# Optimization experiments

Measured on AMD Instinct MI355X. Metric: run time of the kernel, lower is better.

Reference implementation:

```python
import jax, jax.numpy as jnp
import numpy as np
import math

D_MODEL = 1024
N_HEADS = 16
D_K = D_MODEL // N_HEADS
LN_EPS = 1e-5


def _linear_params(key, d_in, d_out):
    # torch Linear stores weight as [out, in]; xavier_uniform init
    bound = math.sqrt(6.0 / (d_in + d_out))
    kw, kb = jax.random.split(key)
    W = jax.random.uniform(kw, (d_out, d_in), jnp.float32, -bound, bound)
    b = jnp.zeros((d_out,), jnp.float32)
    return W, b


def setup_inputs() -> dict:
    key = jax.random.key(0)
    ks = jax.random.split(key, 8)
    x = jax.random.normal(ks[0], (2, 2048, D_MODEL), jnp.float32)
    reasoning_state = jax.random.normal(ks[1], (2, D_MODEL), jnp.float32)
    Wq, bq = _linear_params(ks[2], D_MODEL, D_MODEL)
    Wk, bk = _linear_params(ks[3], D_MODEL, D_MODEL)
    Wv, bv = _linear_params(ks[4], D_MODEL, D_MODEL)
    Wr, br = _linear_params(ks[5], D_MODEL, D_MODEL)
    Wo, bo = _linear_params(ks[6], D_MODEL, D_MODEL)
    ln_g = jnp.ones((D_MODEL,), jnp.float32)
    ln_b = jnp.zeros((D_MODEL,), jnp.float32)
    return {"x": x, "reasoning_state": reasoning_state,
            "Wq": Wq, "bq": bq, "Wk": Wk, "bk": bk, "Wv": Wv, "bv": bv,
            "Wr": Wr, "br": br, "Wo": Wo, "bo": bo, "ln_g": ln_g, "ln_b": ln_b}


def reference(x, reasoning_state, Wq, bq, Wk, bk, Wv, bv, Wr, br, Wo, bo, ln_g, ln_b):
    B, S, D = x.shape
    H, dk = N_HEADS, D_K

    def proj(z, W, b):  # torch Linear: z @ W.T + b
        return z @ W.T + b

    # [B, H, S, dk]
    Q = proj(x, Wq, bq).reshape(B, S, H, dk).transpose(0, 2, 1, 3)
    K = proj(x, Wk, bk).reshape(B, S, H, dk).transpose(0, 2, 1, 3)
    V = proj(x, Wv, bv).reshape(B, S, H, dk).transpose(0, 2, 1, 3)

    scores = jnp.einsum('bhsd,bhtd->bhst', Q, K) / math.sqrt(dk)

    # reasoning bias: R is [B, H, 1, dk]; Q @ R^T -> [B, H, S, 1], broadcast over keys
    R = proj(reasoning_state, Wr, br).reshape(B, 1, H, dk).transpose(0, 2, 1, 3)
    scores = scores + jnp.einsum('bhsd,bhud->bhsu', Q, R)  # u == 1, broadcasts

    attn = jax.nn.softmax(scores, axis=-1)
    context = jnp.einsum('bhst,bhtd->bshd', attn, V).reshape(B, S, D)
    out = proj(context, Wo, bo)

    # residual + LayerNorm
    y = out + x
    mu = jnp.mean(y, axis=-1, keepdims=True)
    var = jnp.var(y, axis=-1, keepdims=True)
    y = (y - mu) * jax.lax.rsqrt(var + LN_EPS) * ln_g + ln_b
    return (y, attn)
```

## Files before the change

### kernel.cpp

```cpp
#include <hip/hip_runtime.h>
#include <hip/hip_bf16.h>

#define DM 1024
#define NH 16
#define DKK 64
#define SL 2048
#define NBATCH 2
#define NR (NBATCH*SL)

typedef __attribute__((ext_vector_type(8))) __bf16 bf16x8;
typedef __attribute__((ext_vector_type(4))) float f32x4;
using bf16 = __hip_bfloat16;

#define QSCALE 0.18033688011112042f

__global__ __launch_bounds__(256) void cvt5_kernel(
    const float* __restrict__ sx, const float* __restrict__ s1,
    const float* __restrict__ s2, const float* __restrict__ s3, const float* __restrict__ s4,
    bf16* __restrict__ dx, bf16* __restrict__ d1,
    bf16* __restrict__ d2, bf16* __restrict__ d3, bf16* __restrict__ d4) {
  const int z = blockIdx.y;
  const float* src = (z == 0) ? sx : (z == 1) ? s1 : (z == 2) ? s2 : (z == 3) ? s3 : s4;
  bf16* dst = (z == 0) ? dx : (z == 1) ? d1 : (z == 2) ? d2 : (z == 3) ? d3 : d4;
  const int n4 = (z == 0) ? (NR * DM / 4) : (DM * DM / 4);
  int stride = gridDim.x * blockDim.x;
  for (int i = blockIdx.x * blockDim.x + threadIdx.x; i < n4; i += stride) {
    float4 v = ((const float4*)src)[i];
    union { bf16 h[4]; ushort4 u; } un;
    un.h[0] = __float2bfloat16(v.x);
    un.h[1] = __float2bfloat16(v.y);
    un.h[2] = __float2bfloat16(v.z);
    un.h[3] = __float2bfloat16(v.w);
    ((ushort4*)dst)[i] = un.u;
  }
}

__device__ __forceinline__ void gemm_core(const bf16* __restrict__ A, const bf16* __restrict__ W,
                                          int rowStart, int colStart,
                                          bf16* As, bf16* Bs, f32x4 acc[4][4]) {
  const int t = threadIdx.x;
  const int lane = t & 63, w = t >> 6;
  const int lg = lane & 15, lh = lane >> 4;
  const int wm = (w >> 1) * 64, wn = (w & 1) * 64;
#pragma unroll
  for (int i = 0; i < 4; ++i)
#pragma unroll
    for (int j = 0; j < 4; ++j) acc[i][j] = (f32x4){0.f, 0.f, 0.f, 0.f};

  for (int kt = 0; kt < DM / 32; ++kt) {
    int kb = kt * 32;
#pragma unroll
    for (int q = 0; q < 2; ++q) {
      int idx = q * 256 + t;
      int row = idx >> 2;
      int ce = (idx & 3) * 8;
      const bf16* ga = A + (size_t)(rowStart + row) * DM + kb + ce;
      const bf16* gb = W + (size_t)(colStart + row) * DM + kb + ce;
      int ldsbase = (q * 256 + w * 64) * 8;
      __builtin_amdgcn_global_load_lds((const __attribute__((address_space(1))) void*)ga,
                                       (__attribute__((address_space(3))) void*)(As + ldsbase),
                                       16, 0, 0);
      __builtin_amdgcn_global_load_lds((const __attribute__((address_space(1))) void*)gb,
                                       (__attribute__((address_space(3))) void*)(Bs + ldsbase),
                                       16, 0, 0);
    }
    __syncthreads();
    bf16x8 af[4], bfr[4];
#pragma unroll
    for (int i = 0; i < 4; ++i)
      af[i] = *(const bf16x8*)(As + (wm + i * 16 + lg) * 32 + 8 * lh);
#pragma unroll
    for (int j = 0; j < 4; ++j)
      bfr[j] = *(const bf16x8*)(Bs + (wn + j * 16 + lg) * 32 + 8 * lh);
#pragma unroll
    for (int i = 0; i < 4; ++i)
#pragma unroll
      for (int j = 0; j < 4; ++j)
        acc[i][j] = __builtin_amdgcn_mfma_f32_16x16x32_bf16(af[i], bfr[j], acc[i][j], 0, 0, 0);
    __syncthreads();
  }
}

__global__ __launch_bounds__(256) void gemm_qkv_kernel(
    const bf16* __restrict__ xb,
    const bf16* __restrict__ Wqb, const bf16* __restrict__ Wkb, const bf16* __restrict__ Wvb,
    const float* __restrict__ bq, const float* __restrict__ bk, const float* __restrict__ bv,
    bf16* __restrict__ Qb, bf16* __restrict__ Kb, bf16* __restrict__ Vt) {
  __shared__ bf16 smem[128 * 128];
  bf16* As = smem;
  bf16* Bs = smem + 4096;
  const int z = blockIdx.z;
  const bf16* W = (z == 0) ? Wqb : (z == 1) ? Wkb : Wvb;
  const float* bias = (z == 0) ? bq : (z == 1) ? bk : bv;
  int rowStart = blockIdx.y * 128, colStart = blockIdx.x * 128;
  f32x4 acc[4][4];
  gemm_core(xb, W, rowStart, colStart, As, Bs, acc);

  const int t = threadIdx.x, lane = t & 63, w = t >> 6;
  const int lg = lane & 15, lh = lane >> 4;
  const int wm = (w >> 1) * 64, wn = (w & 1) * 64;
  if (z < 2) {
    bf16* out = (z == 0) ? Qb : Kb;
    const float sc = (z == 0) ? QSCALE : 1.0f;
#pragma unroll
    for (int i = 0; i < 4; ++i)
#pragma unroll
      for (int j = 0; j < 4; ++j) {
        int col = colStart + wn + j * 16 + lg;
        float bb = bias[col];
#pragma unroll
        for (int r = 0; r < 4; ++r) {
          int row = rowStart + wm + i * 16 + 4 * lh + r;
          out[(size_t)row * DM + col] = __float2bfloat16((acc[i][j][r] + bb) * sc);
        }
      }
  } else {
    char* T = (char*)smem;
    __syncthreads();
#pragma unroll
    for (int i = 0; i < 4; ++i)
#pragma unroll
      for (int j = 0; j < 4; ++j) {
        int col = wn + j * 16 + lg;
        float bb = bias[colStart + col];
        const int swz = (col & 7) << 4;
#pragma unroll
        for (int r2 = 0; r2 < 4; r2 += 2) {
          int row = wm + i * 16 + 4 * lh + r2;
          union { bf16 hh[2]; unsigned u; } un;
          un.hh[0] = __float2bfloat16(acc[i][j][r2] + bb);
          un.hh[1] = __float2bfloat16(acc[i][j][r2 + 1] + bb);
          *(unsigned*)(T + ((col * 256 + row * 2) ^ swz)) = un.u;
        }
      }
    __syncthreads();
    const int b_i = rowStart >> 11;
    const int sbase = rowStart & 2047;
#pragma unroll
    for (int rd = 0; rd < 8; ++rd) {
      int d_loc = rd * 16 + (t >> 4);
      int s8 = (t & 15) * 8;
      bf16x8 v = *(const bf16x8*)(T + ((d_loc * 256 + s8 * 2) ^ ((d_loc & 7) << 4)));
      int col = colStart + d_loc;
      int h2 = col >> 6, d = col & 63;
      *(bf16x8*)(Vt + ((size_t)(b_i * NH + h2) * DKK + d) * SL + sbase + s8) = v;
    }
  }
}

__global__ __launch_bounds__(256) void attn_den_kernel(
    const bf16* __restrict__ Qb, const bf16* __restrict__ Kb,
    float* __restrict__ linv_g) {
  __shared__ float sl[2 * 128];
  const int t = threadIdx.x, lane = t & 63, w = t >> 6;
  const int lg = lane & 15, lh = lane >> 4;
  const int L = blockIdx.x;
  const int xcd = L & 7, s_in = L >> 3;
  const int bh = xcd * 4 + (s_in >> 4);
  const int qtile = s_in & 15;
  const int b = bh >> 4, h = bh & 15;
  const int qbase = qtile * 128;
  const int wr = w >> 1, wc = w & 1;

  bf16x8 qf[4][2];
#pragma unroll
  for (int i = 0; i < 4; ++i)
#pragma unroll
    for (int ks = 0; ks < 2; ++ks)
      qf[i][ks] = *(const bf16x8*)(Qb +
          (size_t)(b * SL + qbase + wr * 64 + i * 16 + lg) * DM + h * DKK + ks * 32 + 8 * lh);

  const bf16* Kbase = Kb + (size_t)b * SL * DM + h * DKK;

  float lsum[4] = {0.f, 0.f, 0.f, 0.f};
  for (int kt = 0; kt < 16; ++kt) {
    bf16x8 kf[4][2];
#pragma unroll
    for (int j = 0; j < 4; ++j)
#pragma unroll
      for (int ks = 0; ks < 2; ++ks)
        kf[j][ks] = *(const bf16x8*)(Kbase +
            (size_t)(kt * 128 + wc * 64 + j * 16 + lg) * DM + ks * 32 + 8 * lh);
#pragma unroll
    for (int i = 0; i < 4; ++i) {
      f32x4 s[4];
#pragma unroll
      for (int j = 0; j < 4; ++j) {
        f32x4 z = (f32x4){0.f, 0.f, 0.f, 0.f};
        z = __builtin_amdgcn_mfma_f32_16x16x32_bf16(kf[j][0], qf[i][0], z, 0, 0, 0);
        s[j] = __builtin_amdgcn_mfma_f32_16x16x32_bf16(kf[j][1], qf[i][1], z, 0, 0, 0);
      }
#pragma unroll
      for (int j = 0; j < 4; ++j)
#pragma unroll
        for (int r = 0; r < 4; ++r) lsum[i] += exp2f(s[j][r]);
    }
  }
#pragma unroll
  for (int i = 0; i < 4; ++i) {
    lsum[i] += __shfl_xor(lsum[i], 16);
    lsum[i] += __shfl_xor(lsum[i], 32);
  }
  if (lh == 0) {
#pragma unroll
    for (int i = 0; i < 4; ++i) sl[wc * 128 + wr * 64 + i * 16 + lg] = lsum[i];
  }
  __syncthreads();
  if (t < 128) {
    linv_g[(size_t)bh * SL + qbase + t] = 1.f / (sl[t] + sl[128 + t]);
  }
}

__global__ __launch_bounds__(256) void attn_wr_kernel(
    const bf16* __restrict__ Qb, const bf16* __restrict__ Kb, const bf16* __restrict__ Vt,
    const float* __restrict__ linv_g,
    float* __restrict__ attn_out, bf16* __restrict__ ctxb) {
  __shared__ bf16 Ps[4][2][32 * 128];
  const int t = threadIdx.x, lane = t & 63, w = t >> 6;
  const int lg = lane & 15, lh = lane >> 4;
  const int L = blockIdx.x;
  const int xcd = L & 7, s_in = L >> 3;
  const int bh = xcd * 4 + (s_in >> 4);
  const int qtile = s_in & 15;
  const int b = bh >> 4, h = bh & 15;
  const int qb2 = qtile * 128 + w * 32;
  char* Pw = (char*)(&Ps[w][0][0]);

  bf16x8 qf[2][2];
#pragma unroll
  for (int i = 0; i < 2; ++i)
#pragma unroll
    for (int ks = 0; ks < 2; ++ks)
      qf[i][ks] = *(const bf16x8*)(Qb +
          (size_t)(b * SL + qb2 + i * 16 + lg) * DM + h * DKK + ks * 32 + 8 * lh);

  float linv[2];
#pragma unroll
  for (int i = 0; i < 2; ++i)
    linv[i] = linv_g[(size_t)bh * SL + qb2 + i * 16 + lg];

  const bf16* Kbase = Kb + (size_t)b * SL * DM + h * DKK;
  const bf16* Vtb = Vt + (size_t)bh * DKK * SL;
  float* attn_base = attn_out + (size_t)bh * SL * SL;

  f32x4 cacc[2][4];
#pragma unroll
  for (int i = 0; i < 2; ++i)
#pragma unroll
    for (int jd = 0; jd < 4; ++jd) cacc[i][jd] = (f32x4){0.f, 0.f, 0.f, 0.f};

  for (int kt = 0; kt < 16; ++kt) {
    char* Pb = Pw + (kt & 1) * 8192;
    bf16x8 kf[8][2];
#pragma unroll
    for (int j = 0; j < 8; ++j)
#pragma unroll
      for (int ks = 0; ks < 2; ++ks)
        kf[j][ks] = *(const bf16x8*)(Kbase +
            (size_t)(kt * 128 + j * 16 + lg) * DM + ks * 32 + 8 * lh);
    bf16x8 vfall[4][4];
#pragma unroll
    for (int ks = 0; ks < 4; ++ks)
#pragma unroll
      for (int jd = 0; jd < 4; ++jd)
        vfall[ks][jd] = *(const bf16x8*)(Vtb +
            (size_t)(jd * 16 + lg) * SL + kt * 128 + ks * 32 + 8 * lh);

#pragma unroll
    for (int i = 0; i < 2; ++i) {
      f32x4 s[8];
      __builtin_amdgcn_s_setprio(1);
#pragma unroll
      for (int j = 0; j < 8; ++j) {
        f32x4 z = (f32x4){0.f, 0.f, 0.f, 0.f};
        z = __builtin_amdgcn_mfma_f32_16x16x32_bf16(kf[j][0], qf[i][0], z, 0, 0, 0);
        s[j] = __builtin_amdgcn_mfma_f32_16x16x32_bf16(kf[j][1], qf[i][1], z, 0, 0, 0);
      }
      __builtin_amdgcn_s_setprio(0);
      const int qloc = i * 16 + lg;
      const int swz = (qloc & 7) << 4;
#pragma unroll
      for (int j = 0; j < 8; ++j) {
        const int key0 = j * 16 + 4 * lh;
        f32x4 p4;
        p4[0] = exp2f(s[j][0]) * linv[i];
        p4[1] = exp2f(s[j][1]) * linv[i];
        p4[2] = exp2f(s[j][2]) * linv[i];
        p4[3] = exp2f(s[j][3]) * linv[i];
        __builtin_nontemporal_store(p4,
            (f32x4*)(attn_base + (size_t)(qb2 + qloc) * SL + kt * 128 + key0));
        union { bf16 hh[4]; ushort4 u4; } un;
        un.hh[0] = __float2bfloat16(p4[0]);
        un.hh[1] = __float2bfloat16(p4[1]);
        un.hh[2] = __float2bfloat16(p4[2]);
        un.hh[3] = __float2bfloat16(p4[3]);
        *(ushort4*)(Pb + ((qloc * 256 + key0 * 2) ^ swz)) = un.u4;
      }
    }

    __builtin_amdgcn_s_setprio(1);
#pragma unroll
    for (int ks = 0; ks < 4; ++ks) {
      bf16x8 pf[2];
#pragma unroll
      for (int i = 0; i < 2; ++i) {
        const int qloc = i * 16 + lg;
        pf[i] = *(const bf16x8*)(Pb + ((qloc * 256 + (ks * 32 + 8 * lh) * 2) ^ ((qloc & 7) << 4)));
      }
#pragma unroll
      for (int i = 0; i < 2; ++i)
#pragma unroll
        for (int jd = 0; jd < 4; ++jd)
          cacc[i][jd] = __builtin_amdgcn_mfma_f32_16x16x32_bf16(pf[i], vfall[ks][jd], cacc[i][jd], 0, 0, 0);
    }
    __builtin_amdgcn_s_setprio(0);
  }

#pragma unroll
  for (int i = 0; i < 2; ++i)
#pragma unroll
    for (int jd = 0; jd < 4; ++jd)
#pragma unroll
      for (int r = 0; r < 4; ++r) {
        int row = qb2 + i * 16 + 4 * lh + r;
        int d = jd * 16 + lg;
        ctxb[(size_t)(b * SL + row) * DM + h * DKK + d] = __float2bfloat16(cacc[i][jd][r]);
      }
}

__global__ __launch_bounds__(256) void gemm_o_kernel(
    const bf16* __restrict__ ctxb, const bf16* __restrict__ Wob, const float* __restrict__ bo,
    const float* __restrict__ xf, float* __restrict__ ypre) {
  __shared__ bf16 As[128 * 32], Bs[64 * 32];
  const int t = threadIdx.x, lane = t & 63, w = t >> 6;
  const int lg = lane & 15, lh = lane >> 4;
  const int wm = (w >> 1) * 64, wn = (w & 1) * 32;
  int rowStart = blockIdx.y * 128, colStart = blockIdx.x * 64;
  f32x4 acc[4][2];
#pragma unroll
  for (int i = 0; i < 4; ++i)
#pragma unroll
    for (int j = 0; j < 2; ++j) acc[i][j] = (f32x4){0.f, 0.f, 0.f, 0.f};

  for (int kt = 0; kt < DM / 32; ++kt) {
    int kb = kt * 32;
#pragma unroll
    for (int q = 0; q < 2; ++q) {
      int idx = q * 256 + t;
      int row = idx >> 2;
      int ce = (idx & 3) * 8;
      const bf16* ga = ctxb + (size_t)(rowStart + row) * DM + kb + ce;
      int ldsbase = (q * 256 + w * 64) * 8;
      __builtin_amdgcn_global_load_lds((const __attribute__((address_space(1))) void*)ga,
                                       (__attribute__((address_space(3))) void*)(As + ldsbase),
                                       16, 0, 0);
    }
    {
      int row = t >> 2, ce = (t & 3) * 8;
      const bf16* gb = Wob + (size_t)(colStart + row) * DM + kb + ce;
      int ldsbase = (w * 64) * 8;
      __builtin_amdgcn_global_load_lds((const __attribute__((address_space(1))) void*)gb,
                                       (__attribute__((address_space(3))) void*)(Bs + ldsbase),
                                       16, 0, 0);
    }
    __syncthreads();
    bf16x8 af[4], bfr[2];
#pragma unroll
    for (int i = 0; i < 4; ++i)
      af[i] = *(const bf16x8*)(As + (wm + i * 16 + lg) * 32 + 8 * lh);
#pragma unroll
    for (int j = 0; j < 2; ++j)
      bfr[j] = *(const bf16x8*)(Bs + (wn + j * 16 + lg) * 32 + 8 * lh);
#pragma unroll
    for (int i = 0; i < 4; ++i)
#pragma unroll
      for (int j = 0; j < 2; ++j)
        acc[i][j] = __builtin_amdgcn_mfma_f32_16x16x32_bf16(af[i], bfr[j], acc[i][j], 0, 0, 0);
    __syncthreads();
  }
#pragma unroll
  for (int i = 0; i < 4; ++i)
#pragma unroll
    for (int j = 0; j < 2; ++j) {
      int col = colStart + wn + j * 16 + lg;
      float bb = bo[col];
#pragma unroll
      for (int r = 0; r < 4; ++r) {
        int row = rowStart + wm + i * 16 + 4 * lh + r;
        ypre[(size_t)row * DM + col] = acc[i][j][r] + bb + xf[(size_t)row * DM + col];
      }
    }
}

__global__ __launch_bounds__(256) void ln_kernel(const float* __restrict__ ypre,
                                                 const float* __restrict__ g,
                                                 const float* __restrict__ bta,
                                                 float* __restrict__ out) {
  int row = blockIdx.x;
  const float* yr = ypre + (size_t)row * DM;
  int t = threadIdx.x;
  float4 v = *(const float4*)(yr + t * 4);
  float s = v.x + v.y + v.z + v.w;
  float ss = v.x * v.x + v.y * v.y + v.z * v.z + v.w * v.w;
#pragma unroll
  for (int off = 1; off < 64; off <<= 1) {
    s += __shfl_xor(s, off);
    ss += __shfl_xor(ss, off);
  }
  __shared__ float red[8];
  int w = t >> 6, lane = t & 63;
  if (lane == 0) { red[w] = s; red[4 + w] = ss; }
  __syncthreads();
  s = red[0] + red[1] + red[2] + red[3];
  ss = red[4] + red[5] + red[6] + red[7];
  float mu = s * (1.f / (float)DM);
  float var = ss * (1.f / (float)DM) - mu * mu;
  float rstd = rsqrtf(var + 1e-5f);
  float4 gv = *(const float4*)(g + t * 4);
  float4 bv = *(const float4*)(bta + t * 4);
  float4 o;
  o.x = (v.x - mu) * rstd * gv.x + bv.x;
  o.y = (v.y - mu) * rstd * gv.y + bv.y;
  o.z = (v.z - mu) * rstd * gv.z + bv.z;
  o.w = (v.w - mu) * rstd * gv.w + bv.w;
  *(float4*)(out + (size_t)row * DM + t * 4) = o;
}

extern "C" void kernel_launch(void* const* d_in, const int* in_sizes, int n_in,
                              void* d_out, int out_size, void* d_ws, size_t ws_size,
                              hipStream_t stream) {
  (void)in_sizes; (void)n_in; (void)out_size; (void)ws_size;
  const float* x = (const float*)d_in[0];
  const float* Wq = (const float*)d_in[2];
  const float* bq = (const float*)d_in[3];
  const float* Wk = (const float*)d_in[4];
  const float* bk = (const float*)d_in[5];
  const float* Wv = (const float*)d_in[6];
  const float* bv = (const float*)d_in[7];
  const float* Wo = (const float*)d_in[10];
  const float* bo = (const float*)d_in[11];
  const float* ln_g = (const float*)d_in[12];
  const float* ln_b = (const float*)d_in[13];
  float* out = (float*)d_out;

  char* ws = (char*)d_ws;
  const size_t MB = 1ull << 20;
  bf16* xb   = (bf16*)(ws + 0 * MB);
  bf16* Wqb  = (bf16*)(ws + 8 * MB);
  bf16* Wkb  = (bf16*)(ws + 10 * MB);
  bf16* Wvb  = (bf16*)(ws + 12 * MB);
  bf16* Wob  = (bf16*)(ws + 14 * MB);
  bf16* Qb   = (bf16*)(ws + 16 * MB);
  bf16* Kb   = (bf16*)(ws + 24 * MB);
  bf16* Vt   = (bf16*)(ws + 32 * MB);
  bf16* ctxb = (bf16*)(ws + 40 * MB);
  float* ypre = (float*)(ws + 48 * MB);
  float* linv_g = (float*)(ws + 64 * MB);

  float* y_out = out;
  float* attn_out = out + (size_t)NR * DM;

  cvt5_kernel<<<dim3(512, 5), 256, 0, stream>>>(x, Wq, Wk, Wv, Wo, xb, Wqb, Wkb, Wvb, Wob);

  gemm_qkv_kernel<<<dim3(8, 32, 3), 256, 0, stream>>>(xb, Wqb, Wkb, Wvb, bq, bk, bv, Qb, Kb, Vt);
  attn_den_kernel<<<512, 256, 0, stream>>>(Qb, Kb, linv_g);
  attn_wr_kernel<<<512, 256, 0, stream>>>(Qb, Kb, Vt, linv_g, attn_out, ctxb);
  gemm_o_kernel<<<dim3(16, 32), 256, 0, stream>>>(ctxb, Wob, bo, x, ypre);
  ln_kernel<<<4096, 256, 0, stream>>>(ypre, ln_g, ln_b, y_out);
}
```

Before: 304.8 us.

## Halve per-wave query rows in attention-write kernel and double-buffer K fragment loads

Each wave in the attention-write kernel now handles 16 query rows instead of 32, and the grid doubles to 1024 blocks. K fragments are loaded in pairs with a double buffer inside the key tile, and V fragments are loaded per k-slice rather than all up front. The aim is to cut register pressure and raise occupancy so the large attention-matrix stores overlap better with compute. The cost is that K and V tiles are reloaded twice as often across blocks, and fewer MFMAs are issued per load.

Result: slower. 371.5 us (+21.9%).

```diff
diff --git a/kernel.cpp b/kernel.cpp
--- a/kernel.cpp
+++ b/kernel.cpp
@@ -215,117 +215,100 @@
     const bf16* __restrict__ Qb, const bf16* __restrict__ Kb, const bf16* __restrict__ Vt,
     const float* __restrict__ linv_g,
     float* __restrict__ attn_out, bf16* __restrict__ ctxb) {
-  __shared__ bf16 Ps[4][2][32 * 128];
+  __shared__ bf16 Ps[4][2][16 * 128];
   const int t = threadIdx.x, lane = t & 63, w = t >> 6;
   const int lg = lane & 15, lh = lane >> 4;
   const int L = blockIdx.x;
   const int xcd = L & 7, s_in = L >> 3;
-  const int bh = xcd * 4 + (s_in >> 4);
-  const int qtile = s_in & 15;
+  const int bh = xcd * 4 + (s_in >> 5);
+  const int qtile = s_in & 31;
   const int b = bh >> 4, h = bh & 15;
-  const int qb2 = qtile * 128 + w * 32;
+  const int qb2 = qtile * 64 + w * 16;
   char* Pw = (char*)(&Ps[w][0][0]);
 
-  bf16x8 qf[2][2];
-#pragma unroll
-  for (int i = 0; i < 2; ++i)
-#pragma unroll
-    for (int ks = 0; ks < 2; ++ks)
-      qf[i][ks] = *(const bf16x8*)(Qb +
-          (size_t)(b * SL + qb2 + i * 16 + lg) * DM + h * DKK + ks * 32 + 8 * lh);
-
-  float linv[2];
-#pragma unroll
-  for (int i = 0; i < 2; ++i)
-    linv[i] = linv_g[(size_t)bh * SL + qb2 + i * 16 + lg];
+  bf16x8 qf[2];
+#pragma unroll
+  for (int ks = 0; ks < 2; ++ks)
+    qf[ks] = *(const bf16x8*)(Qb +
+        (size_t)(b * SL + qb2 + lg) * DM + h * DKK + ks * 32 + 8 * lh);
+
+  const float linv = linv_g[(size_t)bh * SL + qb2 + lg];
 
   const bf16* Kbase = Kb + (size_t)b * SL * DM + h * DKK;
   const bf16* Vtb = Vt + (size_t)bh * DKK * SL;
   float* attn_base = attn_out + (size_t)bh * SL * SL;
 
-  f32x4 cacc[2][4];
-#pragma unroll
-  for (int i = 0; i < 2; ++i)
-#pragma unroll
-    for (int jd = 0; jd < 4; ++jd) cacc[i][jd] = (f32x4){0.f, 0.f, 0.f, 0.f};
+  f32x4 cacc[4];
+#pragma unroll
+  for (int jd = 0; jd < 4; ++jd) cacc[jd] = (f32x4){0.f, 0.f, 0.f, 0.f};
 
   for (int kt = 0; kt < 16; ++kt) {
-    char* Pb = Pw + (kt & 1) * 8192;
-    bf16x8 kf[8][2];
-#pragma unroll
-    for (int j = 0; j < 8; ++j)
+    char* Pb = Pw + (kt & 1) * 4096;
+    bf16x8 kf[2][2][2];
+#pragma unroll
+    for (int jj = 0; jj < 2; ++jj)
 #pragma unroll
       for (int ks = 0; ks < 2; ++ks)
-        kf[j][ks] = *(const bf16x8*)(Kbase +
-            (size_t)(kt * 128 + j * 16 + lg) * DM + ks * 32 + 8 * lh);
-    bf16x8 vfall[4][4];
-#pragma unroll
-    for (int ks = 0; ks < 4; ++ks)
-#pragma unroll
-      for (int jd = 0; jd < 4; ++jd)
-        vfall[ks][jd] = *(const bf16x8*)(Vtb +
-            (size_t)(jd * 16 + lg) * SL + kt * 128 + ks * 32 + 8 * lh);
-
-#pragma unroll
-    for (int i = 0; i < 2; ++i) {
-      f32x4 s[8];
-      __builtin_amdgcn_s_setprio(1);
-#pragma unroll
-      for (int j = 0; j < 8; ++j) {
+        kf[0][jj][ks] = *(const bf16x8*)(Kbase +
+            (size_t)(kt * 128 + jj * 16 + lg) * DM + ks * 32 + 8 * lh);
+#pragma unroll
+    for (int jp = 0; jp < 4; ++jp) {
+      const int cur = jp & 1, nxt = cur ^ 1;
+      if (jp < 3) {
+#pragma unroll
+        for (int jj = 0; jj < 2; ++jj)
+#pragma unroll
+          for (int ks = 0; ks < 2; ++ks)
+            kf[nxt][jj][ks] = *(const bf16x8*)(Kbase +
+                (size_t)(kt * 128 + (jp + 1) * 32 + jj * 16 + lg) * DM + ks * 32 + 8 * lh);
+      }
+#pragma unroll
+      for (int jj = 0; jj < 2; ++jj) {
+        const int j = jp * 2 + jj;
         f32x4 z = (f32x4){0.f, 0.f, 0.f, 0.f};
-        z = __builtin_amdgcn_mfma_f32_16x16x32_bf16(kf[j][0], qf[i][0], z, 0, 0, 0);
-        s[j] = __builtin_amdgcn_mfma_f32_16x16x32_bf16(kf[j][1], qf[i][1], z, 0, 0, 0);
-      }
-      __builtin_amdgcn_s_setprio(0);
-      const int qloc = i * 16 + lg;
-      const int swz = (qloc & 7) << 4;
-#pragma unroll
-      for (int j = 0; j < 8; ++j) {
-        const int key0 = j * 16 + 4 * lh;
+        z = __builtin_amdgcn_mfma_f32_16x16x32_bf16(kf[cur][jj][0], qf[0], z, 0, 0, 0);
+        f32x4 s = __builtin_amdgcn_mfma_f32_16x16x32_bf16(kf[cur][jj][1], qf[1], z, 0, 0, 0);
         f32x4 p4;
-        p4[0] = exp2f(s[j][0]) * linv[i];
-        p4[1] = exp2f(s[j][1]) * linv[i];
-        p4[2] = exp2f(s[j][2]) * linv[i];
-        p4[3] = exp2f(s[j][3]) * linv[i];
+        p4[0] = exp2f(s[0]) * linv;
+        p4[1] = exp2f(s[1]) * linv;
+        p4[2] = exp2f(s[2]) * linv;
+        p4[3] = exp2f(s[3]) * linv;
         __builtin_nontemporal_store(p4,
-            (f32x4*)(attn_base + (size_t)(qb2 + qloc) * SL + kt * 128 + key0));
+            (f32x4*)(attn_base + (size_t)(qb2 + lg) * SL + kt * 128 + j * 16 + 4 * lh));
         union { bf16 hh[4]; ushort4 u4; } un;
         un.hh[0] = __float2bfloat16(p4[0]);
         un.hh[1] = __float2bfloat16(p4[1]);
         un.hh[2] = __float2bfloat16(p4[2]);
         un.hh[3] = __float2bfloat16(p4[3]);
-        *(ushort4*)(Pb + ((qloc * 256 + key0 * 2) ^ swz)) = un.u4;
-      }
-    }
-
-    __builtin_amdgcn_s_setprio(1);
+        *(ushort4*)(Pb + ((lg * 256 + (j * 16 + 4 * lh) * 2) ^ ((lg & 7) << 4))) = un.u4;
+      }
+    }
+
 #pragma unroll
     for (int ks = 0; ks < 4; ++ks) {
-      bf16x8 pf[2];
-#pragma unroll
-      for (int i = 0; i < 2; ++i) {
-        const int qloc = i * 16 + lg;
-        pf[i] = *(const bf16x8*)(Pb + ((qloc * 256 + (ks * 32 + 8 * lh) * 2) ^ ((qloc & 7) << 4)));
-      }
-#pragma unroll
-      for (int i = 0; i < 2; ++i)
-#pragma unroll
-        for (int jd = 0; jd < 4; ++jd)
-          cacc[i][jd] = __builtin_amdgcn_mfma_f32_16x16x32_bf16(pf[i], vfall[ks][jd], cacc[i][jd], 0, 0, 0);
-    }
-    __builtin_amdgcn_s_setprio(0);
-  }
-
-#pragma unroll
-  for (int i = 0; i < 2; ++i)
-#pragma unroll
-    for (int jd = 0; jd < 4; ++jd)
-#pragma unroll
-      for (int r = 0; r < 4; ++r) {
-        int row = qb2 + i * 16 + 4 * lh + r;
-        int d = jd * 16 + lg;
-        ctxb[(size_t)(b * SL + row) * DM + h * DKK + d] = __float2bfloat16(cacc[i][jd][r]);
-      }
+      bf16x8 pf = *(const bf16x8*)(Pb +
+          ((lg * 256 + (ks * 32 + 8 * lh) * 2) ^ ((lg & 7) << 4)));
+      bf16x8 vf[4];
+#pragma unroll
+      for (int jd = 0; jd < 4; ++jd)
+        vf[jd] = *(const bf16x8*)(Vtb +
+            (size_t)(jd * 16 + lg) * SL + kt * 128 + ks * 32 + 8 * lh);
+      __builtin_amdgcn_s_setprio(1);
+#pragma unroll
+      for (int jd = 0; jd < 4; ++jd)
+        cacc[jd] = __builtin_amdgcn_mfma_f32_16x16x32_bf16(pf, vf[jd], cacc[jd], 0, 0, 0);
+      __builtin_amdgcn_s_setprio(0);
+    }
+  }
+
+#pragma unroll
+  for (int jd = 0; jd < 4; ++jd)
+#pragma unroll
+    for (int r = 0; r < 4; ++r) {
+      int row = qb2 + 4 * lh + r;
+      int d = jd * 16 + lg;
+      ctxb[(size_t)(b * SL + row) * DM + h * DKK + d] = __float2bfloat16(cacc[jd][r]);
+    }
 }
 
 __global__ __launch_bounds__(256) void gemm_o_kernel(
@@ -464,7 +447,7 @@
 
   gemm_qkv_kernel<<<dim3(8, 32, 3), 256, 0, stream>>>(xb, Wqb, Wkb, Wvb, bq, bk, bv, Qb, Kb, Vt);
   attn_den_kernel<<<512, 256, 0, stream>>>(Qb, Kb, linv_g);
-  attn_wr_kernel<<<512, 256, 0, stream>>>(Qb, Kb, Vt, linv_g, attn_out, ctxb);
+  attn_wr_kernel<<<1024, 256, 0, stream>>>(Qb, Kb, Vt, linv_g, attn_out, ctxb);
   gemm_o_kernel<<<dim3(16, 32), 256, 0, stream>>>(ctxb, Wob, bo, x, ypre);
   ln_kernel<<<4096, 256, 0, stream>>>(ypre, ln_g, ln_b, y_out);
 }
```
